# Optimization experiments

Measured on AMD Instinct MI355X. Metric: run time of the kernel, lower is better.

## Reference

```python
import jax, jax.numpy as jnp
import numpy as np

B, S, D, H, HD, W, DFF = 2, 8192, 768, 12, 64, 256, 3072
NEG = -1e9


def ln(x, s, b, eps):
    m = jnp.mean(x, axis=-1, keepdims=True)
    v = jnp.mean((x - m) ** 2, axis=-1, keepdims=True)
    return (x - m) / jnp.sqrt(v + eps) * s + b


def band_attn(q, k, v, w):
    # q,k,v: [B,H,S,HD]; q already scaled by 1/sqrt(HD).
    b, h, s, d = q.shape
    nc = s // w  # non-overlapping query chunks of size w
    qc = q.reshape(b, h, nc, w, d)
    pad = ((0, 0), (0, 0), (w, w), (0, 0))
    kp = jnp.pad(k, pad)
    vp = jnp.pad(v, pad)
    # key chunk c covers global positions [c*w - w, c*w + 2w) -> length 3w
    idx = jnp.arange(nc)[:, None] * w + jnp.arange(3 * w)[None, :]  # [nc,3w]
    kc = kp[:, :, idx]  # [B,H,nc,3w,HD]
    vc = vp[:, :, idx]
    scores = jnp.einsum('bhcqd,bhckd->bhcqk', qc, kc)  # [B,H,nc,w,3w]
    # relative offset key-query: key global = c*w - w + j, query global = c*w + i
    rel = jnp.arange(3 * w)[None, :] - w - jnp.arange(w)[:, None]  # [w,3w]
    band = jnp.abs(rel) <= w
    kpos = jnp.arange(nc)[:, None] * w - w + jnp.arange(3 * w)[None, :]  # [nc,3w]
    valid = (kpos >= 0) & (kpos < s)
    mask = band[None, :, :] & valid[:, None, :]  # [nc,w,3w]
    scores = jnp.where(mask, scores, NEG)
    probs = jax.nn.softmax(scores, axis=-1)
    out = jnp.einsum('bhcqk,bhckd->bhcqd', probs, vc)
    return out.reshape(b, h, s, d)


def longformer_layer(hidden, pos_emb, tt_emb, emb_ln_s, emb_ln_b,
                     wq, bq, wk, bk, wv, bv, wo, bo, attn_ln_s, attn_ln_b,
                     wi, bi, wo2, bo2, out_ln_s, out_ln_b):
    # embeddings: inputs_embeds + position + token_type(0), LN eps 1e-12
    h = ln(hidden + pos_emb[None, :hidden.shape[1]] + tt_emb, emb_ln_s, emb_ln_b, 1e-12)
    def heads(x):
        return x.reshape(B, S, H, HD).transpose(0, 2, 1, 3)
    q = heads(h @ wq + bq) / jnp.sqrt(jnp.float32(HD))
    k = heads(h @ wk + bk)
    v = heads(h @ wv + bv)
    a = band_attn(q, k, v, W)  # [B,H,S,HD]
    a = a.transpose(0, 2, 1, 3).reshape(B, S, D)
    h2 = ln(h + (a @ wo + bo), attn_ln_s, attn_ln_b, 1e-12)
    inter = jax.nn.gelu(h2 @ wi + bi, approximate=False)
    return ln(h2 + (inter @ wo2 + bo2), out_ln_s, out_ln_b, 1e-12)


def setup_inputs() -> dict:
    key = jax.random.key(0)
    ks = jax.random.split(key, 16)
    wn = lambda k, shp: jax.random.normal(k, shp, jnp.float32) * 0.02
    d = {
        'src': jax.random.normal(ks[0], (B, S, D), jnp.float32),
        'pos_emb': wn(ks[1], (S, D)),
        'tt_emb': wn(ks[2], (D,)),
        'emb_ln_s': jnp.ones((D,)), 'emb_ln_b': jnp.zeros((D,)),
        'wq': wn(ks[3], (D, D)), 'bq': jnp.zeros((D,)),
        'wk': wn(ks[4], (D, D)), 'bk': jnp.zeros((D,)),
        'wv': wn(ks[5], (D, D)), 'bv': jnp.zeros((D,)),
        'wo': wn(ks[6], (D, D)), 'bo': jnp.zeros((D,)),
        'attn_ln_s': jnp.ones((D,)), 'attn_ln_b': jnp.zeros((D,)),
        'wi': wn(ks[7], (D, DFF)), 'bi': jnp.zeros((DFF,)),
        'wo2': wn(ks[8], (DFF, D)), 'bo2': jnp.zeros((D,)),
        'out_ln_s': jnp.ones((D,)), 'out_ln_b': jnp.zeros((D,)),
        'n1_s': jnp.ones((D,)), 'n1_b': jnp.zeros((D,)),
        'n2_s': jnp.ones((D,)), 'n2_b': jnp.zeros((D,)),
        'w1': wn(ks[9], (D, DFF)), 'b1': jnp.zeros((DFF,)),
        'w2': wn(ks[10], (DFF, D)), 'b2': jnp.zeros((D,)),
    }
    return d


def reference(src, pos_emb, tt_emb, emb_ln_s, emb_ln_b, wq, bq, wk, bk, wv, bv,
              wo, bo, attn_ln_s, attn_ln_b, wi, bi, wo2, bo2, out_ln_s, out_ln_b,
              n1_s, n1_b, n2_s, n2_b, w1, b1, w2, b2):
    hidden = ln(src, n1_s, n1_b, 1e-5)
    out = longformer_layer(hidden, pos_emb, tt_emb, emb_ln_s, emb_ln_b,
                           wq, bq, wk, bk, wv, bv, wo, bo, attn_ln_s, attn_ln_b,
                           wi, bi, wo2, bo2, out_ln_s, out_ln_b)
    src2 = src + out  # dropout is identity in eval
    ff = jax.nn.relu(ln(src2, n2_s, n2_b, 1e-5) @ w1 + b1)
    ff = ff @ w2 + b2
    return src2 + ff
```

## Files before the change

kernel.cpp:

```cpp
#include <hip/hip_runtime.h>

#define SLEN 8192
#define BD   768
#define NH   12
#define NTOK 16384
#define HTOK 8192

typedef __bf16 bf16;
typedef __bf16 bf16x8 __attribute__((ext_vector_type(8)));
typedef float  floatx4 __attribute__((ext_vector_type(4)));

#define MFMA16(a, b, c) __builtin_amdgcn_mfma_f32_16x16x32_bf16((a), (b), (c), 0, 0, 0)

__device__ __forceinline__ int iclamp(int v, int lo, int hi) {
  return v < lo ? lo : (v > hi ? hi : v);
}

__device__ __forceinline__ void gl2lds16(const bf16* g, bf16* l) {
  __builtin_amdgcn_global_load_lds(
      (const __attribute__((address_space(1))) void*)g,
      (__attribute__((address_space(3))) void*)l,
      16, 0, 0);
}

__global__ __launch_bounds__(256) void k_prep_w(const float* __restrict__ W,
                                                bf16* __restrict__ Wt,
                                                int K, int N, float scale) {
  __shared__ float tile[32][33];
  const int tid = threadIdx.x;
  const int tx = tid & 31, ty = tid >> 5;
  const int n0 = blockIdx.x * 32, k0 = blockIdx.y * 32;
#pragma unroll
  for (int i = 0; i < 32; i += 8)
    tile[ty + i][tx] = W[(size_t)(k0 + ty + i) * N + n0 + tx];
  __syncthreads();
#pragma unroll
  for (int i = 0; i < 32; i += 8)
    Wt[(size_t)(n0 + ty + i) * K + k0 + tx] = (bf16)(tile[tx][ty + i] * scale);
}

__global__ void k_prep_qkv_bias(const float* __restrict__ bq, const float* __restrict__ bk,
                                const float* __restrict__ bv, float* __restrict__ out) {
  int i = blockIdx.x * 256 + threadIdx.x;
  if (i < 768) out[i] = bq[i] * 0.125f;
  else if (i < 1536) out[i] = bk[i - 768];
  else if (i < 2304) out[i] = bv[i - 1536];
}

__device__ __forceinline__ float block_sum768(float v, float* red) {
#pragma unroll
  for (int off = 32; off > 0; off >>= 1) v += __shfl_down(v, off);
  __syncthreads();
  if ((threadIdx.x & 63) == 0) red[threadIdx.x >> 6] = v;
  __syncthreads();
  return red[0] + red[1] + red[2] + red[3];
}

__global__ __launch_bounds__(256) void k_ln_ln_emb(const float* __restrict__ src,
    const float* __restrict__ pos, const float* __restrict__ tt,
    const float* __restrict__ s1, const float* __restrict__ b1,
    const float* __restrict__ s2, const float* __restrict__ b2,
    float* __restrict__ hf, bf16* __restrict__ hb) {
  __shared__ float red[4];
  const int tid = threadIdx.x;
  const size_t row = blockIdx.x;
  const int sp = blockIdx.x & (SLEN - 1);
  const float* x = src + row * BD;
  float v0 = x[tid], v1 = x[tid + 256], v2 = x[tid + 512];
  const float mean = block_sum768(v0 + v1 + v2, red) * (1.f / 768.f);
  v0 -= mean; v1 -= mean; v2 -= mean;
  const float var = block_sum768(v0 * v0 + v1 * v1 + v2 * v2, red) * (1.f / 768.f);
  const float rstd = rsqrtf(var + 1e-5f);
  const float* pr = pos + (size_t)sp * BD;
  float y0 = v0 * rstd * s1[tid]       + b1[tid]       + pr[tid]       + tt[tid];
  float y1 = v1 * rstd * s1[tid + 256] + b1[tid + 256] + pr[tid + 256] + tt[tid + 256];
  float y2 = v2 * rstd * s1[tid + 512] + b1[tid + 512] + pr[tid + 512] + tt[tid + 512];
  const float mean2 = block_sum768(y0 + y1 + y2, red) * (1.f / 768.f);
  y0 -= mean2; y1 -= mean2; y2 -= mean2;
  const float var2 = block_sum768(y0 * y0 + y1 * y1 + y2 * y2, red) * (1.f / 768.f);
  const float rstd2 = rsqrtf(var2 + 1e-12f);
  float o0 = y0 * rstd2 * s2[tid]       + b2[tid];
  float o1 = y1 * rstd2 * s2[tid + 256] + b2[tid + 256];
  float o2 = y2 * rstd2 * s2[tid + 512] + b2[tid + 512];
  float* hr = hf + row * BD;
  bf16* hbr = hb + row * BD;
  hr[tid] = o0; hr[tid + 256] = o1; hr[tid + 512] = o2;
  hbr[tid] = (bf16)o0; hbr[tid + 256] = (bf16)o1; hbr[tid + 512] = (bf16)o2;
}

__global__ __launch_bounds__(256) void k_ln(const float* __restrict__ x,
    const float* __restrict__ s, const float* __restrict__ b, float eps,
    float* __restrict__ of, bf16* __restrict__ ob) {
  __shared__ float red[4];
  const int tid = threadIdx.x;
  const size_t row = blockIdx.x;
  const float* xr = x + row * BD;
  float v0 = xr[tid], v1 = xr[tid + 256], v2 = xr[tid + 512];
  const float mean = block_sum768(v0 + v1 + v2, red) * (1.f / 768.f);
  v0 -= mean; v1 -= mean; v2 -= mean;
  const float var = block_sum768(v0 * v0 + v1 * v1 + v2 * v2, red) * (1.f / 768.f);
  const float rstd = rsqrtf(var + eps);
  float o0 = v0 * rstd * s[tid] + b[tid];
  float o1 = v1 * rstd * s[tid + 256] + b[tid + 256];
  float o2 = v2 * rstd * s[tid + 512] + b[tid + 512];
  float* ofr = of + row * BD; bf16* obr = ob + row * BD;
  ofr[tid] = o0; ofr[tid + 256] = o1; ofr[tid + 512] = o2;
  obr[tid] = (bf16)o0; obr[tid + 256] = (bf16)o1; obr[tid + 512] = (bf16)o2;
}

__global__ __launch_bounds__(256) void k_ln_add_ln(const float* __restrict__ y,
    const float* __restrict__ src,
    const float* __restrict__ so, const float* __restrict__ bo_,
    const float* __restrict__ s2, const float* __restrict__ b2,
    float* __restrict__ src2, bf16* __restrict__ tb) {
  __shared__ float red[4];
  const int tid = threadIdx.x;
  const size_t row = blockIdx.x;
  const float* xr = y + row * BD;
  float v0 = xr[tid], v1 = xr[tid + 256], v2 = xr[tid + 512];
  const float mean = block_sum768(v0 + v1 + v2, red) * (1.f / 768.f);
  v0 -= mean; v1 -= mean; v2 -= mean;
  const float var = block_sum768(v0 * v0 + v1 * v1 + v2 * v2, red) * (1.f / 768.f);
  const float rstd = rsqrtf(var + 1e-12f);
  const float* sr = src + row * BD;
  float u0 = sr[tid]       + v0 * rstd * so[tid]       + bo_[tid];
  float u1 = sr[tid + 256] + v1 * rstd * so[tid + 256] + bo_[tid + 256];
  float u2 = sr[tid + 512] + v2 * rstd * so[tid + 512] + bo_[tid + 512];
  float* s2r = src2 + row * BD;
  s2r[tid] = u0; s2r[tid + 256] = u1; s2r[tid + 512] = u2;
  const float mean2 = block_sum768(u0 + u1 + u2, red) * (1.f / 768.f);
  u0 -= mean2; u1 -= mean2; u2 -= mean2;
  const float var2 = block_sum768(u0 * u0 + u1 * u1 + u2 * u2, red) * (1.f / 768.f);
  const float rstd2 = rsqrtf(var2 + 1e-5f);
  bf16* tr = tb + row * BD;
  tr[tid]       = (bf16)(u0 * rstd2 * s2[tid]       + b2[tid]);
  tr[tid + 256] = (bf16)(u1 * rstd2 * s2[tid + 256] + b2[tid + 256]);
  tr[tid + 512] = (bf16)(u2 * rstd2 * s2[tid + 512] + b2[tid + 512]);
}

template <int ACT, bool RES, bool OUTB>
__global__ __launch_bounds__(256, 2) void k_gemm(const bf16* __restrict__ A,
                                                 const bf16* __restrict__ Bt,
                                                 const float* __restrict__ bias,
                                                 const float* __restrict__ resid,
                                                 float* __restrict__ Cf,
                                                 bf16* __restrict__ Cb,
                                                 int M, int N, int K) {
  __shared__ __align__(16) bf16 As[128 * 32];
  __shared__ __align__(16) bf16 Bs[128 * 32];
  const int tid = threadIdx.x;
  const int lane = tid & 63, wave = tid >> 6;
  const int quad = lane >> 4, c = lane & 15;
  const int wr = wave >> 1, wc = wave & 1;
  const int n0 = blockIdx.x * 128, m0 = blockIdx.y * 128;

  const int rA0 = wave * 32 + (lane >> 2);
  const int rA1 = rA0 + 16;
  const int gch = (((lane & 3) ^ ((lane >> 3) & 3)) << 3);
  const bf16* gA0 = A  + (size_t)(m0 + rA0) * K + gch;
  const bf16* gA1 = A  + (size_t)(m0 + rA1) * K + gch;
  const bf16* gB0 = Bt + (size_t)(n0 + rA0) * K + gch;
  const bf16* gB1 = Bt + (size_t)(n0 + rA1) * K + gch;
  bf16* lA0 = As + wave * 1024;
  bf16* lA1 = As + wave * 1024 + 512;
  bf16* lB0 = Bs + wave * 1024;
  bf16* lB1 = Bs + wave * 1024 + 512;

  const int xorq = ((quad ^ ((c >> 1) & 3)) << 3);
  const bf16* aRd[4];
  const bf16* bRd[4];
#pragma unroll
  for (int i = 0; i < 4; ++i) {
    aRd[i] = As + (wr * 64 + i * 16 + c) * 32 + xorq;
    bRd[i] = Bs + (wc * 64 + i * 16 + c) * 32 + xorq;
  }

  floatx4 acc[4][4];
#pragma unroll
  for (int i = 0; i < 4; ++i)
#pragma unroll
    for (int j = 0; j < 4; ++j) acc[i][j] = floatx4{0.f, 0.f, 0.f, 0.f};

  for (int k0 = 0; k0 < K; k0 += 32) {
    __syncthreads();
    gl2lds16(gA0 + k0, lA0);
    gl2lds16(gA1 + k0, lA1);
    gl2lds16(gB0 + k0, lB0);
    gl2lds16(gB1 + k0, lB1);
    __syncthreads();
    bf16x8 af[4], bfv[4];
#pragma unroll
    for (int i = 0; i < 4; ++i) af[i] = *(const bf16x8*)aRd[i];
#pragma unroll
    for (int j = 0; j < 4; ++j) bfv[j] = *(const bf16x8*)bRd[j];
#pragma unroll
    for (int i = 0; i < 4; ++i)
#pragma unroll
      for (int j = 0; j < 4; ++j)
        acc[i][j] = MFMA16(af[i], bfv[j], acc[i][j]);
  }

  const int rbase = m0 + wr * 64 + quad * 4;
  const int cbase = n0 + wc * 64 + c;
#pragma unroll
  for (int i = 0; i < 4; ++i) {
#pragma unroll
    for (int j = 0; j < 4; ++j) {
      const int col = cbase + j * 16;
      const float bc = bias[col];
#pragma unroll
      for (int r = 0; r < 4; ++r) {
        const int row = rbase + i * 16 + r;
        float v = acc[i][j][r] + bc;
        if (RES) v += resid[(size_t)row * N + col];
        if (ACT == 1) v = 0.5f * v * (1.f + erff(v * 0.70710678118654752f));
        if (ACT == 2) v = fmaxf(v, 0.f);
        if (OUTB) Cb[(size_t)row * N + col] = (bf16)v;
        else      Cf[(size_t)row * N + col] = v;
      }
    }
  }
}

__global__ __launch_bounds__(256) void k_vtrans(const bf16* __restrict__ qkv_b, bf16* __restrict__ vt) {
  __shared__ bf16 tile[64][72];
  const int tid = threadIdx.x;
  const int blk = blockIdx.x;
  const int h  = blk >> 7;
  const int st = blk & 127;
  const int s0 = st * 64;
  {
    const int d = tid & 63, si4 = tid >> 6;
    const bf16* src = qkv_b + (size_t)s0 * 2304 + 1536 + h * 64 + d;
#pragma unroll
    for (int i = 0; i < 16; ++i) {
      int s = si4 * 16 + i;
      tile[s][d] = src[(size_t)s * 2304];
    }
  }
  __syncthreads();
  {
    const int s = tid & 63, di4 = tid >> 6;
#pragma unroll
    for (int i = 0; i < 16; ++i) {
      int d = di4 * 16 + i;
      vt[((size_t)(h * 64 + d)) * SLEN + s0 + s] = tile[s][d];
    }
  }
}

__global__ __launch_bounds__(256, 4) void k_attn(const bf16* __restrict__ qkv_b,
                                                 const bf16* __restrict__ vt,
                                                 bf16* __restrict__ aout_b) {
  __shared__ __align__(16) bf16 Ks[2][64 * 64];
  __shared__ __align__(16) bf16 Vs[2][64 * 64];
  __shared__ __align__(16) bf16 Ps[4][16 * 64];
  const int tid  = threadIdx.x;
  const int wave = tid >> 6, lane = tid & 63;
  const int quad = lane >> 4, c = lane & 15;
  const int blk0 = blockIdx.x;
  const int wg   = ((blk0 & 7) * 192) + (blk0 >> 3);
  const int h    = wg >> 7;
  const int st   = wg & 127;
  const int q0b  = st * 64;
  const int q0   = q0b + wave * 16;

  const bf16* qp = qkv_b + (size_t)(q0 + c) * 2304 + h * 64 + quad * 8;
  const bf16x8 aq0 = *(const bf16x8*)(qp);
  const bf16x8 aq1 = *(const bf16x8*)(qp + 32);

  const int srow  = lane >> 3;
  const int chunk = ((lane & 7) ^ srow) << 3;
  const int krow0 = wave * 16 + srow;

  const int xlo = (quad ^ (c & 7)) << 3;
  const int xhi = ((quad + 4) ^ (c & 7)) << 3;

  floatx4 o[4];
  float m[4], l[4];
#pragma unroll
  for (int r = 0; r < 4; ++r) {
    o[r] = floatx4{0.f, 0.f, 0.f, 0.f};
    m[r] = -1e30f; l[r] = 0.f;
  }
  bf16* Pw = &Ps[wave][0];

  const int t_lo = st < 4 ? 4 - st : 0;
  const int t_hi = st > 123 ? 132 - st : 9;

  auto stage = [&](int buf, int t) {
    const int kb  = q0b - 256 + 64 * t;
    const int kr0 = iclamp(kb + krow0, 0, SLEN - 1);
    const int kr1 = iclamp(kb + krow0 + 8, 0, SLEN - 1);
    gl2lds16(qkv_b + (size_t)kr0 * 2304 + 768 + h * 64 + chunk, &Ks[buf][wave * 1024]);
    gl2lds16(qkv_b + (size_t)kr1 * 2304 + 768 + h * 64 + chunk, &Ks[buf][wave * 1024 + 512]);
    const int kbc = iclamp(kb, 0, SLEN - 64);
    gl2lds16(vt + (size_t)(h * 64 + krow0) * SLEN + kbc + chunk, &Vs[buf][wave * 1024]);
    gl2lds16(vt + (size_t)(h * 64 + krow0 + 8) * SLEN + kbc + chunk, &Vs[buf][wave * 1024 + 512]);
  };

  int cur = 0;
  stage(0, t_lo);
  for (int t = t_lo; t < t_hi; ++t) {
    __syncthreads();
    if (t + 1 < t_hi) stage(cur ^ 1, t + 1);
    const int kb = q0b - 256 + 64 * t;
    const bf16* Kb = &Ks[cur][0];
    const bf16* Vb = &Vs[cur][0];

    floatx4 s[4];
#pragma unroll
    for (int i = 0; i < 4; ++i) s[i] = floatx4{0.f, 0.f, 0.f, 0.f};
#pragma unroll
    for (int ks = 0; ks < 4; ++ks) {
      const bf16* kr = Kb + (ks * 16 + c) * 64;
      s[ks] = MFMA16(aq0, *(const bf16x8*)(kr + xlo), s[ks]);
      s[ks] = MFMA16(aq1, *(const bf16x8*)(kr + xhi), s[ks]);
    }
    if (t == 0 || t == 8) {
#pragma unroll
      for (int ks = 0; ks < 4; ++ks)
#pragma unroll
        for (int r = 0; r < 4; ++r) {
          int d = (kb + ks * 16 + c) - (q0 + quad * 4 + r);
          d = d < 0 ? -d : d;
          if (d > 256) s[ks][r] = -INFINITY;
        }
    }

    float tm[4], rs[4];
#pragma unroll
    for (int r = 0; r < 4; ++r)
      tm[r] = fmaxf(fmaxf(s[0][r], s[1][r]), fmaxf(s[2][r], s[3][r]));
#pragma unroll
    for (int off = 1; off < 16; off <<= 1)
#pragma unroll
      for (int r = 0; r < 4; ++r) tm[r] = fmaxf(tm[r], __shfl_xor(tm[r], off));
#pragma unroll
    for (int r = 0; r < 4; ++r) {
      const float mn = fmaxf(m[r], tm[r]);
      const float al = __expf(m[r] - mn);
      m[r] = mn;
      float sum = 0.f;
#pragma unroll
      for (int ks = 0; ks < 4; ++ks) { s[ks][r] = __expf(s[ks][r] - mn); sum += s[ks][r]; }
      rs[r] = sum;
      l[r] *= al;
#pragma unroll
      for (int n = 0; n < 4; ++n) o[n][r] *= al;
    }
#pragma unroll
    for (int off = 1; off < 16; off <<= 1)
#pragma unroll
      for (int r = 0; r < 4; ++r) rs[r] += __shfl_xor(rs[r], off);
#pragma unroll
    for (int r = 0; r < 4; ++r) l[r] += rs[r];

#pragma unroll
    for (int ks = 0; ks < 4; ++ks)
#pragma unroll
      for (int r = 0; r < 4; ++r) {
        const int prow = quad * 4 + r;
        const int col  = ks * 16 + c;
        Pw[prow * 64 + ((((col >> 3) ^ (prow & 7)) << 3) | (col & 7))] = (bf16)s[ks][r];
      }
    asm volatile("s_waitcnt lgkmcnt(0)" ::: "memory");
    const bf16x8 pa0 = *(const bf16x8*)(Pw + c * 64 + xlo);
    const bf16x8 pa1 = *(const bf16x8*)(Pw + c * 64 + xhi);
#pragma unroll
    for (int n = 0; n < 4; ++n) {
      const bf16* vr = Vb + (n * 16 + c) * 64;
      o[n] = MFMA16(pa0, *(const bf16x8*)(vr + xlo), o[n]);
      o[n] = MFMA16(pa1, *(const bf16x8*)(vr + xhi), o[n]);
    }
    cur ^= 1;
  }

#pragma unroll
  for (int r = 0; r < 4; ++r) {
    const float inv = 1.f / l[r];
    const size_t orow = (size_t)(q0 + quad * 4 + r) * BD + h * 64;
#pragma unroll
    for (int n = 0; n < 4; ++n)
      aout_b[orow + n * 16 + c] = (bf16)(o[n][r] * inv);
  }
}

extern "C" void kernel_launch(void* const* d_in, const int* in_sizes, int n_in,
                              void* d_out, int out_size, void* d_ws, size_t ws_size,
                              hipStream_t stream) {
  (void)in_sizes; (void)n_in; (void)out_size; (void)ws_size;
  const float* src     = (const float*)d_in[0];
  const float* pos_emb = (const float*)d_in[1];
  const float* tt_emb  = (const float*)d_in[2];
  const float* emb_s   = (const float*)d_in[3];
  const float* emb_b   = (const float*)d_in[4];
  const float* wq      = (const float*)d_in[5];
  const float* bq      = (const float*)d_in[6];
  const float* wk      = (const float*)d_in[7];
  const float* bk      = (const float*)d_in[8];
  const float* wv      = (const float*)d_in[9];
  const float* bv      = (const float*)d_in[10];
  const float* wo      = (const float*)d_in[11];
  const float* bo      = (const float*)d_in[12];
  const float* atn_s   = (const float*)d_in[13];
  const float* atn_b   = (const float*)d_in[14];
  const float* wi      = (const float*)d_in[15];
  const float* bi      = (const float*)d_in[16];
  const float* wo2     = (const float*)d_in[17];
  const float* bo2     = (const float*)d_in[18];
  const float* out_s   = (const float*)d_in[19];
  const float* out_b   = (const float*)d_in[20];
  const float* n1_s    = (const float*)d_in[21];
  const float* n1_b    = (const float*)d_in[22];
  const float* n2_s    = (const float*)d_in[23];
  const float* n2_b    = (const float*)d_in[24];
  const float* w1      = (const float*)d_in[25];
  const float* b1      = (const float*)d_in[26];
  const float* w2      = (const float*)d_in[27];
  const float* b2      = (const float*)d_in[28];

  char* ws = (char*)d_ws;
  size_t off = 0;
  auto alloc = [&](size_t bytes) {
    char* p = ws + off;
    off += (bytes + 255) & ~(size_t)255;
    return p;
  };

  bf16* qkvt  = (bf16*)alloc((size_t)2304 * 768 * 2);
  bf16* wot   = (bf16*)alloc((size_t)768 * 768 * 2);
  bf16* wit   = (bf16*)alloc((size_t)3072 * 768 * 2);
  bf16* wo2t  = (bf16*)alloc((size_t)768 * 3072 * 2);
  bf16* w1t   = (bf16*)alloc((size_t)3072 * 768 * 2);
  bf16* w2t   = (bf16*)alloc((size_t)768 * 3072 * 2);
  float* qkvb = (float*)alloc((size_t)2304 * 4);
  char* R1 = alloc((size_t)NTOK * BD * 4);
  char* R2 = alloc((size_t)NTOK * BD * 2);
  char* R3 = alloc((size_t)HTOK * 2304 * 2
                 + (size_t)NH * 64 * SLEN * 2
                 + (size_t)HTOK * BD * 2);

  float* h_f   = (float*)R1;
  bf16*  hb    = (bf16*)R2;
  bf16*  qkvB  = (bf16*)R3;
  bf16*  vtB   = (bf16*)(R3 + (size_t)HTOK * 2304 * 2);
  bf16*  aoutB = (bf16*)(R3 + (size_t)HTOK * 2304 * 2 + (size_t)NH * 64 * SLEN * 2);
  float* y1    = (float*)d_out;
  float* h2f   = (float*)R1;
  bf16*  h2b   = (bf16*)R2;
  bf16*  interC= (bf16*)R3;
  float* y2    = (float*)d_out;
  float* src2  = (float*)R1;
  bf16*  tb    = (bf16*)R2;
  bf16*  ff1C  = (bf16*)R3;
  float* outp  = (float*)d_out;

  dim3 blk(256);
  k_prep_w<<<dim3(24, 24), blk, 0, stream>>>(wq, qkvt,                 768, 768, 0.125f);
  k_prep_w<<<dim3(24, 24), blk, 0, stream>>>(wk, qkvt + 768 * 768,     768, 768, 1.f);
  k_prep_w<<<dim3(24, 24), blk, 0, stream>>>(wv, qkvt + 2 * 768 * 768, 768, 768, 1.f);
  k_prep_w<<<dim3(24, 24), blk, 0, stream>>>(wo, wot,                  768, 768, 1.f);
  k_prep_w<<<dim3(96, 24), blk, 0, stream>>>(wi, wit,    768, 3072, 1.f);
  k_prep_w<<<dim3(24, 96), blk, 0, stream>>>(wo2, wo2t, 3072, 768,  1.f);
  k_prep_w<<<dim3(96, 24), blk, 0, stream>>>(w1, w1t,    768, 3072, 1.f);
  k_prep_w<<<dim3(24, 96), blk, 0, stream>>>(w2, w2t,   3072, 768,  1.f);
  k_prep_qkv_bias<<<dim3(9), blk, 0, stream>>>(bq, bk, bv, qkvb);

  k_ln_ln_emb<<<dim3(NTOK), blk, 0, stream>>>(src, pos_emb, tt_emb, n1_s, n1_b,
                                              emb_s, emb_b, h_f, hb);
  for (int b = 0; b < 2; ++b) {
    const size_t tok0 = (size_t)b * HTOK;
    k_gemm<0, false, true><<<dim3(18, 64), blk, 0, stream>>>(
        hb + tok0 * BD, qkvt, qkvb, nullptr, nullptr, qkvB, HTOK, 2304, 768);
    k_vtrans<<<dim3(NH * 128), blk, 0, stream>>>(qkvB, vtB);
    k_attn<<<dim3(NH * 128), blk, 0, stream>>>(qkvB, vtB, aoutB);
    k_gemm<0, true, false><<<dim3(6, 64), blk, 0, stream>>>(
        aoutB, wot, bo, h_f + tok0 * BD, y1 + tok0 * BD, nullptr, HTOK, 768, 768);
  }
  k_ln<<<dim3(NTOK), blk, 0, stream>>>(y1, atn_s, atn_b, 1e-12f, h2f, h2b);
  for (int cchunk = 0; cchunk < 2; ++cchunk) {
    const size_t tok0 = (size_t)cchunk * HTOK;
    k_gemm<1, false, true><<<dim3(24, 64), blk, 0, stream>>>(
        h2b + tok0 * BD, wit, bi, nullptr, nullptr, interC, HTOK, 3072, 768);
    k_gemm<0, true, false><<<dim3(6, 64), blk, 0, stream>>>(
        interC, wo2t, bo2, h2f + tok0 * BD, y2 + tok0 * BD, nullptr, HTOK, 768, 3072);
  }
  k_ln_add_ln<<<dim3(NTOK), blk, 0, stream>>>(y2, src, out_s, out_b, n2_s, n2_b, src2, tb);
  for (int cchunk = 0; cchunk < 2; ++cchunk) {
    const size_t tok0 = (size_t)cchunk * HTOK;
    k_gemm<2, false, true><<<dim3(24, 64), blk, 0, stream>>>(
        tb + tok0 * BD, w1t, b1, nullptr, nullptr, ff1C, HTOK, 3072, 768);
    k_gemm<0, true, false><<<dim3(6, 64), blk, 0, stream>>>(
        ff1C, w2t, b2, src2 + tok0 * BD, outp + tok0 * BD, nullptr, HTOK, 768, 3072);
  }
}
```

Baseline: 1.076 ms.

## Double-buffer GEMM LDS tiles and raise occupancy target in launch bounds

The GEMM kernel now keeps two LDS buffers for the A and B tiles and prefetches the next K-slice with global_load_lds while the MFMAs run on the current one. This drops one barrier per iteration and lets global-to-LDS latency overlap with compute. It also raises the launch-bounds occupancy hint from 2 to 4 blocks per CU. That doubles LDS per block and tightens the register budget, which could cause spills or limit how many blocks actually fit.

```diff
diff --git a/kernel.cpp b/kernel.cpp
--- a/kernel.cpp
+++ b/kernel.cpp
@@ -139,15 +139,15 @@
 }
 
 template <int ACT, bool RES, bool OUTB>
-__global__ __launch_bounds__(256, 2) void k_gemm(const bf16* __restrict__ A,
+__global__ __launch_bounds__(256, 4) void k_gemm(const bf16* __restrict__ A,
                                                  const bf16* __restrict__ Bt,
                                                  const float* __restrict__ bias,
                                                  const float* __restrict__ resid,
                                                  float* __restrict__ Cf,
                                                  bf16* __restrict__ Cb,
                                                  int M, int N, int K) {
-  __shared__ __align__(16) bf16 As[128 * 32];
-  __shared__ __align__(16) bf16 Bs[128 * 32];
+  __shared__ __align__(16) bf16 As[2][128 * 32];
+  __shared__ __align__(16) bf16 Bs[2][128 * 32];
   const int tid = threadIdx.x;
   const int lane = tid & 63, wave = tid >> 6;
   const int quad = lane >> 4, c = lane & 15;
@@ -161,18 +161,14 @@
   const bf16* gA1 = A  + (size_t)(m0 + rA1) * K + gch;
   const bf16* gB0 = Bt + (size_t)(n0 + rA0) * K + gch;
   const bf16* gB1 = Bt + (size_t)(n0 + rA1) * K + gch;
-  bf16* lA0 = As + wave * 1024;
-  bf16* lA1 = As + wave * 1024 + 512;
-  bf16* lB0 = Bs + wave * 1024;
-  bf16* lB1 = Bs + wave * 1024 + 512;
+  const int ldst = wave * 1024;
 
   const int xorq = ((quad ^ ((c >> 1) & 3)) << 3);
-  const bf16* aRd[4];
-  const bf16* bRd[4];
+  int aOff[4], bOff[4];
 #pragma unroll
   for (int i = 0; i < 4; ++i) {
-    aRd[i] = As + (wr * 64 + i * 16 + c) * 32 + xorq;
-    bRd[i] = Bs + (wc * 64 + i * 16 + c) * 32 + xorq;
+    aOff[i] = (wr * 64 + i * 16 + c) * 32 + xorq;
+    bOff[i] = (wc * 64 + i * 16 + c) * 32 + xorq;
   }
 
   floatx4 acc[4][4];
@@ -181,23 +177,29 @@
 #pragma unroll
     for (int j = 0; j < 4; ++j) acc[i][j] = floatx4{0.f, 0.f, 0.f, 0.f};
 
+  auto stage = [&](int buf, int k0) {
+    gl2lds16(gA0 + k0, &As[buf][ldst]);
+    gl2lds16(gA1 + k0, &As[buf][ldst + 512]);
+    gl2lds16(gB0 + k0, &Bs[buf][ldst]);
+    gl2lds16(gB1 + k0, &Bs[buf][ldst + 512]);
+  };
+
+  stage(0, 0);
+  int cur = 0;
   for (int k0 = 0; k0 < K; k0 += 32) {
     __syncthreads();
-    gl2lds16(gA0 + k0, lA0);
-    gl2lds16(gA1 + k0, lA1);
-    gl2lds16(gB0 + k0, lB0);
-    gl2lds16(gB1 + k0, lB1);
-    __syncthreads();
+    if (k0 + 32 < K) stage(cur ^ 1, k0 + 32);
     bf16x8 af[4], bfv[4];
 #pragma unroll
-    for (int i = 0; i < 4; ++i) af[i] = *(const bf16x8*)aRd[i];
-#pragma unroll
-    for (int j = 0; j < 4; ++j) bfv[j] = *(const bf16x8*)bRd[j];
+    for (int i = 0; i < 4; ++i) af[i] = *(const bf16x8*)(&As[cur][aOff[i]]);
+#pragma unroll
+    for (int j = 0; j < 4; ++j) bfv[j] = *(const bf16x8*)(&Bs[cur][bOff[j]]);
 #pragma unroll
     for (int i = 0; i < 4; ++i)
 #pragma unroll
       for (int j = 0; j < 4; ++j)
         acc[i][j] = MFMA16(af[i], bfv[j], acc[i][j]);
+    cur ^= 1;
   }
 
   const int rbase = m0 + wr * 64 + quad * 4;
```

New measurement: 1.085 ms. Within noise of the previous version (+0.8%).
